# Kernel optimization log

Hardware: AMD Instinct MI355X
Metric: run time of the kernel (lower is better)

Reference implementation:

```python
import jax, jax.numpy as jnp
import numpy as np

B, N, F, H, L = 2048, 64, 128, 2, 3
Dh = F // H          # feats per head
E = 7                # 3 diff + 1 dist + 3 sigmoid shifts
MAX_SPECIES = 100
SHIFTS = (2.0, 4.0, 6.0)
NEG = -1e9


def layernorm(x):
    # no_upscale_ln: plain normalization, unit scale, zero offset
    m = x.mean(-1, keepdims=True)
    v = x.var(-1, keepdims=True)
    return (x - m) * jax.lax.rsqrt(v + 1e-5)


def featurize(diffs):
    # featurize_real_space_vector with sigmoid_shifts=[2,4,6]
    d = jnp.sqrt((diffs * diffs).sum(-1, keepdims=True) + 1e-12)  # [B,N,N,1]
    sig = jnp.concatenate([jax.nn.sigmoid(d - s) for s in SHIFTS], -1)
    return jnp.concatenate([diffs, d, sig], -1)  # [B,N,N,E]


def setup_inputs() -> dict:
    key = jax.random.key(0)
    ks = jax.random.split(key, 12)
    s = 0.05
    coords = jax.random.normal(ks[0], (B, N, 3), jnp.float32) * 3.0
    species = jax.random.randint(ks[1], (B, N), 1, MAX_SPECIES + 1, jnp.int32)
    lengths = jax.random.randint(ks[2], (B,), N // 2, N + 1)
    mask = jnp.arange(N)[None, :] < lengths[:, None]  # [B,N] bool, padded tails
    return {
        "coords": coords,
        "species": species,
        "mask": mask,
        "embed": jax.random.normal(ks[3], (MAX_SPECIES, F), jnp.float32) * s,
        "Wq": jax.random.normal(ks[4], (L, F, F), jnp.float32) * s,
        "Wk": jax.random.normal(ks[5], (L, F, F), jnp.float32) * s,
        "Wv": jax.random.normal(ks[6], (L, F, F), jnp.float32) * s,
        "Wo": jax.random.normal(ks[7], (L, F, F), jnp.float32) * s,
        "We": jax.random.normal(ks[8], (L, E, H), jnp.float32) * s,
        "Wf": jax.random.normal(ks[9], (L, F, F), jnp.float32) * s,
        "bf": jnp.zeros((L, F), jnp.float32),
    }


def _forward(coords, embed, Wq, Wk, Wv, Wo, We, Wf, bf, species, mask):
    # initial node features from species embedding (species is 1-based)
    h = embed[species - 1] * mask[..., None].astype(embed.dtype)  # [B,N,F]
    nn_mask = mask[:, :, None] & mask[:, None, :]                  # [B,N,N]
    diffs = coords[:, :, None, :] - coords[:, None, :, :]          # [B,N,N,3]
    edges = featurize(diffs) * nn_mask[..., None].astype(coords.dtype)  # [B,N,N,E]
    inv_sqrt_dh = 1.0 / np.sqrt(Dh).astype(np.float32)
    for l in range(L):
        hn = layernorm(h)
        q = (hn @ Wq[l]).reshape(B, N, H, Dh)
        k = (hn @ Wk[l]).reshape(B, N, H, Dh)
        v = (hn @ Wv[l]).reshape(B, N, H, Dh)
        logits = jnp.einsum("bnhd,bmhd->bhnm", q, k) * inv_sqrt_dh
        logits = logits + jnp.einsum("bnme,eh->bhnm", edges, We[l])
        logits = jnp.where(nn_mask[:, None], logits, NEG)
        attn = jax.nn.softmax(logits, axis=-1)                     # [B,H,N,N]
        msg = jnp.einsum("bhnm,bmhd->bnhd", attn, v).reshape(B, N, F)
        h = h + msg @ Wo[l]                                        # attention residual
        h = h + jnp.tanh(layernorm(h) @ Wf[l] + bf[l])             # PsiformerDense residual
        h = h * mask[..., None].astype(h.dtype)
    return layernorm(h)


def reference(coords, species, mask, embed, Wq, Wk, Wv, Wo, We, Wf, bf):
    return _forward(coords, embed, Wq, Wk, Wv, Wo, We, Wf, bf, species, mask)
```

## Files before the change

### kernel.cpp

```cpp
#include <hip/hip_runtime.h>


#define NBATCH 2048
#define NATOM  64
#define NF     128
#define NLAYER 3
#define STR    132
#define ASTRB  136
#define VSTR   72
#define NTH    512

using bf16x8 = __attribute__((ext_vector_type(8))) __bf16;
using bf16x4 = __attribute__((ext_vector_type(4))) __bf16;
using f32x4  = __attribute__((ext_vector_type(4))) float;

__device__ __forceinline__ float bf2f(unsigned short u) {
    union { unsigned int i; float f; } v; v.i = ((unsigned int)u) << 16; return v.f;
}
__device__ __forceinline__ unsigned short f2bf(float f) {
    union { float ff; unsigned int i; } v; v.ff = f;
    unsigned int x = v.i;
    if ((x & 0x7f800000u) == 0x7f800000u) return (unsigned short)(x >> 16);
    return (unsigned short)((x + 0x7fffu + ((x >> 16) & 1u)) >> 16);
}
__device__ __forceinline__ unsigned short bfbits(float x) {
    union { __bf16 b; unsigned short u; } v; v.b = (__bf16)x; return v.u;
}

__device__ __forceinline__ float fast_rcp(float x)  { return __builtin_amdgcn_rcpf(x); }
__device__ __forceinline__ float fast_sqrt(float x) { return __builtin_amdgcn_sqrtf(x); }
__device__ __forceinline__ float fast_exp(float x)  { return __builtin_amdgcn_exp2f(x * 1.4426950408889634f); }

template<bool BF16>
__device__ __forceinline__ float ldT(const void* p, int i) {
    if constexpr (BF16) return bf2f(((const unsigned short*)p)[i]);
    else                return ((const float*)p)[i];
}
template<bool BF16>
__device__ __forceinline__ float4 ld4T(const void* p, int i) {
    if constexpr (BF16) {
        ushort4 v = *(const ushort4*)((const unsigned short*)p + i);
        return make_float4(bf2f(v.x), bf2f(v.y), bf2f(v.z), bf2f(v.w));
    } else {
        return *(const float4*)((const float*)p + i);
    }
}

__device__ __forceinline__ void ln_stats(const float (&h)[4][4], float (&mu)[4], float (&rs)[4]) {
    #pragma unroll
    for (int i = 0; i < 4; ++i) {
        float s  = h[i][0] + h[i][1] + h[i][2] + h[i][3];
        float s2 = h[i][0]*h[i][0] + h[i][1]*h[i][1] + h[i][2]*h[i][2] + h[i][3]*h[i][3];
        #pragma unroll
        for (int m = 1; m <= 16; m <<= 1) {
            s  += __shfl_xor(s,  m);
            s2 += __shfl_xor(s2, m);
        }
        float mm = s * (1.f / 128.f);
        float vv = s2 * (1.f / 128.f) - mm * mm;
        mu[i] = mm;
        rs[i] = rsqrtf(fmaxf(vv, 0.f) + 1e-5f);
    }
}

__device__ __forceinline__ void write_a(const float (&h)[4][4], const float (&mu)[4], const float (&rs)[4],
                                        __bf16* __restrict__ a_hi, int r0, int fq) {
    #pragma unroll
    for (int i = 0; i < 4; ++i) {
        bf16x4 v;
        #pragma unroll
        for (int jj = 0; jj < 4; ++jj)
            v[jj] = (__bf16)((h[i][jj] - mu[i]) * rs[i]);
        *(bf16x4*)&a_hi[(r0 + i) * ASTRB + fq * 4] = v;
    }
}

template<bool WLO>
__device__ __forceinline__ void mfma_dense(const __bf16* __restrict__ a_hi,
                                           const __bf16* __restrict__ bp,
                                           f32x4 (&acc)[2][2], int lane, int wave)
{
    const int R0  = (wave >> 2) << 5;
    const int Cq2 = (wave & 3) << 1;
    const int c = lane & 15, g = lane >> 4;
    const __bf16* bl = bp + 16384;
    #pragma unroll
    for (int t2 = 0; t2 < 2; ++t2)
        #pragma unroll
        for (int j = 0; j < 2; ++j)
            acc[t2][j] = (f32x4){0.f, 0.f, 0.f, 0.f};
    #pragma unroll
    for (int kc = 0; kc < 4; ++kc) {
        const int ao = kc * 32 + (g << 3);
        bf16x8 a0h = *(const bf16x8*)&a_hi[(R0 + c) * ASTRB + ao];
        bf16x8 a1h = *(const bf16x8*)&a_hi[(R0 + 16 + c) * ASTRB + ao];
        #pragma unroll
        for (int j = 0; j < 2; ++j) {
            const int bi = ((((kc << 3) + Cq2 + j) << 6) + lane) << 3;
            bf16x8 bh = *(const bf16x8*)&bp[bi];
            acc[0][j] = __builtin_amdgcn_mfma_f32_16x16x32_bf16(a0h, bh, acc[0][j], 0, 0, 0);
            acc[1][j] = __builtin_amdgcn_mfma_f32_16x16x32_bf16(a1h, bh, acc[1][j], 0, 0, 0);
            if constexpr (WLO) {
                bf16x8 bv = *(const bf16x8*)&bl[bi];
                acc[0][j] = __builtin_amdgcn_mfma_f32_16x16x32_bf16(a0h, bv, acc[0][j], 0, 0, 0);
                acc[1][j] = __builtin_amdgcn_mfma_f32_16x16x32_bf16(a1h, bv, acc[1][j], 0, 0, 0);
            }
        }
    }
}

__device__ __forceinline__ void writeC_rm(const f32x4 (&acc)[2][2],
                                          __bf16* __restrict__ hi, int lane, int wave)
{
    const int R0 = (wave >> 2) << 5;
    const int C0 = (wave & 3) << 5;
    const int c = lane & 15, g4 = (lane >> 4) << 2;
    #pragma unroll
    for (int t2 = 0; t2 < 2; ++t2)
    #pragma unroll
    for (int j = 0; j < 2; ++j)
    #pragma unroll
    for (int r = 0; r < 4; ++r)
        hi[(R0 + 16*t2 + g4 + r) * ASTRB + C0 + 16*j + c] = (__bf16)acc[t2][j][r];
}

__device__ __forceinline__ void writeC_vt(const f32x4 (&acc)[2][2],
                                          __bf16* __restrict__ hi, int lane, int wave)
{
    const int R0 = (wave >> 2) << 5;
    const int C0 = (wave & 3) << 5;
    const int c = lane & 15, g4 = (lane >> 4) << 2;
    #pragma unroll
    for (int t2 = 0; t2 < 2; ++t2)
    #pragma unroll
    for (int j = 0; j < 2; ++j)
    #pragma unroll
    for (int r = 0; r < 4; ++r) {
        int m = R0 + 16*t2 + g4 + r, d = C0 + 16*j + c;
        hi[d * VSTR + m] = (__bf16)acc[t2][j][r];
    }
}

__device__ __forceinline__ void writeC_f32(const f32x4 (&acc)[2][2],
                                           float* __restrict__ dst, int lane, int wave)
{
    const int R0 = (wave >> 2) << 5;
    const int C0 = (wave & 3) << 5;
    const int c = lane & 15, g4 = (lane >> 4) << 2;
    #pragma unroll
    for (int t2 = 0; t2 < 2; ++t2)
    #pragma unroll
    for (int j = 0; j < 2; ++j)
    #pragma unroll
    for (int r = 0; r < 4; ++r)
        dst[(R0 + 16*t2 + g4 + r) * STR + C0 + 16*j + c] = acc[t2][j][r];
}

template<bool BF16>
__global__ __launch_bounds__(256)
void prep_w(const void* __restrict__ Wq, const void* __restrict__ Wk,
            const void* __restrict__ Wv, const void* __restrict__ Wo,
            const void* __restrict__ Wf, unsigned short* __restrict__ wpack)
{
    {
        const unsigned int* w = (const unsigned int*)Wq;
        bool isbf = true;
        #pragma unroll
        for (int i = 0; i < 16; ++i) {
            unsigned int e = (w[i] >> 7) & 0xFFu;
            isbf = isbf && (e >= 0x60u && e <= 0x7Eu);
        }
        if (isbf != BF16) return;
    }
    const int mat  = blockIdx.x;
    const int kind = mat / 3, l = mat % 3;
    const void* src = (kind == 0) ? Wq : (kind == 1) ? Wk : (kind == 2) ? Wv
                    : (kind == 3) ? Wo : Wf;
    unsigned short* dh = wpack + (size_t)mat * 32768;
    unsigned short* dl = dh + 16384;
    for (int f = threadIdx.x; f < 16384; f += 256) {
        int e    = f & 7;
        int lane = (f >> 3) & 63;
        int tj   = (f >> 9) & 7;
        int kc   = f >> 12;
        int row  = kc * 32 + ((lane >> 4) << 3) + e;
        int col  = tj * 16 + (lane & 15);
        float x  = ldT<BF16>(src, (l * NF + row) * NF + col);
        unsigned short hi = f2bf(x);
        unsigned short lo = f2bf(x - bf2f(hi));
        dh[f] = hi; dl[f] = lo;
    }
}

static constexpr size_t SMEM_BYTES =
    (size_t)26624 * 2 + (256 + 48) * 4 + 16;

template<bool BF16>
__global__ __launch_bounds__(NTH, 2)
void gnn_fused(const void* __restrict__ coords,
               const int* __restrict__ species,
               const unsigned char* __restrict__ maskraw,
               const void* __restrict__ embed,
               const void* __restrict__ Wq,
               const void* __restrict__ We,
               const void* __restrict__ bfb,
               const unsigned short* __restrict__ wpack,
               void* __restrict__ out)
{
    constexpr bool WLO = !BF16;
    {
        const unsigned int* w = (const unsigned int*)Wq;
        bool isbf = true;
        #pragma unroll
        for (int i = 0; i < 16; ++i) {
            unsigned int e = (w[i] >> 7) & 0xFFu;
            isbf = isbf && (e >= 0x60u && e <= 0x7Eu);
        }
        if (isbf != BF16) return;
    }

    extern __shared__ __bf16 sm[];
    __bf16* a_hi  = sm;
    __bf16* k_hi  = sm + 8704;
    __bf16* vt_hi = sm + 17408;
    float*  scratch = (float*)k_hi;
    float*  tailf = (float*)(sm + 26624);
    float*  cs   = tailf;
    float*  wel  = cs + 256;
    int*    lenp = (int*)(wel + 48);

    const int t    = threadIdx.x;
    const int b    = blockIdx.x;
    const int fq   = t & 31;
    const int r0   = (t >> 5) * 4;
    const int lane = t & 63;
    const int wave = t >> 6;
    const int c    = lane & 15;
    const int g    = lane >> 4;
    const int g4   = g << 2;
    const int hd   = wave >> 2;
    const int wb   = (wave & 3) << 4;

    if (t < 64) {
        cs[t * 4 + 0] = ldT<BF16>(coords, (b * NATOM + t) * 3 + 0);
        cs[t * 4 + 1] = ldT<BF16>(coords, (b * NATOM + t) * 3 + 1);
        cs[t * 4 + 2] = ldT<BF16>(coords, (b * NATOM + t) * 3 + 2);
    }
    if (t >= 64 && t < 64 + 42) wel[t - 64] = ldT<BF16>(We, t - 64);
    if (t < 64) {
        unsigned int w0 = *(const unsigned int*)maskraw;
        bool f;
        if (w0 == 1u)               f = ((const int*)maskraw)[b * NATOM + t] != 0;
        else if (w0 == 0x01010101u) f = maskraw[b * NATOM + t] != 0;
        else if (w0 == 0x3F800000u) f = ((const float*)maskraw)[b * NATOM + t] != 0.f;
        else                        f = ((const unsigned short*)maskraw)[b * NATOM + t] != 0;
        unsigned long long bal = __ballot(f);
        if (t == 0) *lenp = (int)__popcll(bal);
    }

    float h[4][4];
    #pragma unroll
    for (int i = 0; i < 4; ++i) {
        int sp = species[b * NATOM + r0 + i];
        float4 ev = ld4T<BF16>(embed, (sp - 1) * NF + fq * 4);
        h[i][0] = ev.x; h[i][1] = ev.y; h[i][2] = ev.z; h[i][3] = ev.w;
    }
    __syncthreads();
    const int len = *lenp;
    #pragma unroll
    for (int i = 0; i < 4; ++i)
        if (r0 + i >= len) { h[i][0]=0.f; h[i][1]=0.f; h[i][2]=0.f; h[i][3]=0.f; }

    float mu[4], rs[4];
    for (int l = 0; l < NLAYER; ++l) {
        ln_stats(h, mu, rs);
        write_a(h, mu, rs, a_hi, r0, fq);
        __syncthreads();

        {
            f32x4 kacc[2][2];
            mfma_dense<WLO>(a_hi, (const __bf16*)wpack + (size_t)(3 + l) * 32768, kacc, lane, wave);
            writeC_rm(kacc, k_hi, lane, wave);
        }
        {
            f32x4 vacc[2][2];
            mfma_dense<WLO>(a_hi, (const __bf16*)wpack + (size_t)(6 + l) * 32768, vacc, lane, wave);
            writeC_vt(vacc, vt_hi, lane, wave);
        }
        f32x4 qacc[2][2];
        mfma_dense<WLO>(a_hi, (const __bf16*)wpack + (size_t)(0 + l) * 32768, qacc, lane, wave);
        __syncthreads();
        writeC_rm(qacc, a_hi, lane, wave);
        __syncthreads();

        f32x4 lacc[4];
        #pragma unroll
        for (int jt = 0; jt < 4; ++jt) lacc[jt] = (f32x4){0.f,0.f,0.f,0.f};
        #pragma unroll
        for (int kc = 0; kc < 2; ++kc) {
            const int qo = (wb + c) * ASTRB + hd * 64 + kc * 32 + (g << 3);
            bf16x8 qh = *(const bf16x8*)&a_hi[qo];
            #pragma unroll
            for (int jt = 0; jt < 4; ++jt) {
                const int ko = (jt * 16 + c) * ASTRB + hd * 64 + kc * 32 + (g << 3);
                bf16x8 kh = *(const bf16x8*)&k_hi[ko];
                lacc[jt] = __builtin_amdgcn_mfma_f32_16x16x32_bf16(qh, kh, lacc[jt], 0, 0, 0);
            }
        }
        __syncthreads();

        float we_[7];
        #pragma unroll
        for (int e = 0; e < 7; ++e) we_[e] = wel[l * 14 + e * 2 + hd];
        float cnx[4], cny[4], cnz[4];
        #pragma unroll
        for (int r = 0; r < 4; ++r) {
            int n = wb + g4 + r;
            cnx[r] = cs[n*4]; cny[r] = cs[n*4+1]; cnz[r] = cs[n*4+2];
        }
        float lg[4][4];
        #pragma unroll
        for (int jt = 0; jt < 4; ++jt) {
            int mc = jt * 16 + c;
            float cmx = cs[mc*4], cmy = cs[mc*4+1], cmz = cs[mc*4+2];
            #pragma unroll
            for (int r = 0; r < 4; ++r) {
                float dx = cnx[r]-cmx, dy = cny[r]-cmy, dz = cnz[r]-cmz;
                float d  = fast_sqrt(dx*dx + dy*dy + dz*dz + 1e-12f);
                float et = fast_exp(-d);
                float s1 = fast_rcp(1.f + 7.38905609893065f   * et);
                float s2 = fast_rcp(1.f + 54.598150033144236f * et);
                float s3 = fast_rcp(1.f + 403.4287934927351f  * et);
                lg[jt][r] = lacc[jt][r] * 0.125f
                          + dx*we_[0] + dy*we_[1] + dz*we_[2] + d*we_[3]
                          + s1*we_[4] + s2*we_[5] + s3*we_[6];
            }
        }
        float mx[4] = {-3e38f, -3e38f, -3e38f, -3e38f};
        #pragma unroll
        for (int jt = 0; jt < 4; ++jt)
            if (jt * 16 + c < len) {
                #pragma unroll
                for (int r = 0; r < 4; ++r) mx[r] = fmaxf(mx[r], lg[jt][r]);
            }
        #pragma unroll
        for (int r = 0; r < 4; ++r) {
            mx[r] = fmaxf(mx[r], __shfl_xor(mx[r], 1));
            mx[r] = fmaxf(mx[r], __shfl_xor(mx[r], 2));
            mx[r] = fmaxf(mx[r], __shfl_xor(mx[r], 4));
            mx[r] = fmaxf(mx[r], __shfl_xor(mx[r], 8));
        }
        float sv[4] = {0.f, 0.f, 0.f, 0.f};
        #pragma unroll
        for (int jt = 0; jt < 4; ++jt) {
            bool vm = (jt * 16 + c) < len;
            #pragma unroll
            for (int r = 0; r < 4; ++r) {
                float e = vm ? fast_exp(lg[jt][r] - mx[r]) : 0.f;
                lg[jt][r] = e; sv[r] += e;
            }
        }
        #pragma unroll
        for (int r = 0; r < 4; ++r) {
            sv[r] += __shfl_xor(sv[r], 1);
            sv[r] += __shfl_xor(sv[r], 2);
            sv[r] += __shfl_xor(sv[r], 4);
            sv[r] += __shfl_xor(sv[r], 8);
        }
        float inv[4];
        #pragma unroll
        for (int r = 0; r < 4; ++r)
            inv[r] = (wb + g4 + r < len) ? fast_rcp(sv[r]) : 0.f;

        {
            char* pw = (char*)k_hi + wave * 2048;
            #pragma unroll
            for (int jt = 0; jt < 4; ++jt)
                #pragma unroll
                for (int r = 0; r < 4; ++r) {
                    int x = g4 + r, mm = jt * 16 + c;
                    *(__bf16*)(pw + x * 128 + ((mm * 2) ^ ((x & 7) << 4))) =
                        (__bf16)(lg[jt][r] * inv[r]);
                }
        }

        f32x4 macc[4];
        #pragma unroll
        for (int jt = 0; jt < 4; ++jt) macc[jt] = (f32x4){0.f,0.f,0.f,0.f};
        #pragma unroll
        for (int kc = 0; kc < 2; ++kc) {
            const char* pw = (const char*)k_hi + wave * 2048;
            const int m0 = kc * 32 + (g << 3);
            bf16x8 ph = *(const bf16x8*)(pw + c * 128 + ((m0 * 2) ^ ((c & 7) << 4)));
            #pragma unroll
            for (int jt = 0; jt < 4; ++jt) {
                const int vo = (hd * 64 + jt * 16 + c) * VSTR + kc * 32 + (g << 3);
                bf16x8 vh = *(const bf16x8*)&vt_hi[vo];
                macc[jt] = __builtin_amdgcn_mfma_f32_16x16x32_bf16(ph, vh, macc[jt], 0, 0, 0);
            }
        }
        #pragma unroll
        for (int jt = 0; jt < 4; ++jt)
            #pragma unroll
            for (int r = 0; r < 4; ++r) {
                int idx = (wb + g4 + r) * ASTRB + hd * 64 + jt * 16 + c;
                a_hi[idx] = (__bf16)macc[jt][r];
            }
        __syncthreads();

        {
            f32x4 oacc[2][2];
            mfma_dense<WLO>(a_hi, (const __bf16*)wpack + (size_t)(9 + l) * 32768, oacc, lane, wave);
            writeC_f32(oacc, scratch, lane, wave);
        }
        __syncthreads();
        #pragma unroll
        for (int i = 0; i < 4; ++i) {
            float4 ov = *(const float4*)&scratch[(r0 + i) * STR + fq * 4];
            h[i][0] += ov.x; h[i][1] += ov.y; h[i][2] += ov.z; h[i][3] += ov.w;
        }

        ln_stats(h, mu, rs);
        write_a(h, mu, rs, a_hi, r0, fq);
        __syncthreads();
        {
            f32x4 facc[2][2];
            mfma_dense<WLO>(a_hi, (const __bf16*)wpack + (size_t)(12 + l) * 32768, facc, lane, wave);
            writeC_f32(facc, scratch, lane, wave);
        }
        __syncthreads();
        {
            float4 bv = ld4T<BF16>(bfb, l * NF + fq * 4);
            #pragma unroll
            for (int i = 0; i < 4; ++i) {
                float z0 = scratch[(r0 + i) * STR + fq * 4 + 0] + bv.x;
                float z1 = scratch[(r0 + i) * STR + fq * 4 + 1] + bv.y;
                float z2 = scratch[(r0 + i) * STR + fq * 4 + 2] + bv.z;
                float z3 = scratch[(r0 + i) * STR + fq * 4 + 3] + bv.w;
                h[i][0] += 1.f - 2.f * fast_rcp(fast_exp(2.f*z0) + 1.f);
                h[i][1] += 1.f - 2.f * fast_rcp(fast_exp(2.f*z1) + 1.f);
                h[i][2] += 1.f - 2.f * fast_rcp(fast_exp(2.f*z2) + 1.f);
                h[i][3] += 1.f - 2.f * fast_rcp(fast_exp(2.f*z3) + 1.f);
            }
        }
        #pragma unroll
        for (int i = 0; i < 4; ++i)
            if (r0 + i >= len) { h[i][0]=0.f; h[i][1]=0.f; h[i][2]=0.f; h[i][3]=0.f; }
    }

    ln_stats(h, mu, rs);
    #pragma unroll
    for (int i = 0; i < 4; ++i) {
        int idx = b * NATOM * NF + (r0 + i) * NF + fq * 4;
        float o0 = (h[i][0]-mu[i])*rs[i], o1 = (h[i][1]-mu[i])*rs[i];
        float o2 = (h[i][2]-mu[i])*rs[i], o3 = (h[i][3]-mu[i])*rs[i];
        if constexpr (BF16) {
            ushort4 o;
            o.x = bfbits(o0); o.y = bfbits(o1); o.z = bfbits(o2); o.w = bfbits(o3);
            *(ushort4*)((unsigned short*)out + idx) = o;
        } else {
            *(float4*)((float*)out + idx) = make_float4(o0, o1, o2, o3);
        }
    }
}

extern "C" void kernel_launch(void* const* d_in, const int* in_sizes, int n_in,
                              void* d_out, int out_size, void* d_ws, size_t ws_size,
                              hipStream_t stream) {
    const void*           coords  = d_in[0];
    const int*            species = (const int*)d_in[1];
    const unsigned char*  maskraw = (const unsigned char*)d_in[2];
    const void*           embed   = d_in[3];
    const void*           Wq      = d_in[4];
    const void*           Wk      = d_in[5];
    const void*           Wv      = d_in[6];
    const void*           Wo      = d_in[7];
    const void*           We      = d_in[8];
    const void*           Wf      = d_in[9];
    const void*           bfb     = d_in[10];

    unsigned short* wpack = (unsigned short*)d_ws;

    (void)hipFuncSetAttribute((const void*)gnn_fused<true>,
                              hipFuncAttributeMaxDynamicSharedMemorySize,
                              (int)SMEM_BYTES);
    (void)hipFuncSetAttribute((const void*)gnn_fused<false>,
                              hipFuncAttributeMaxDynamicSharedMemorySize,
                              (int)SMEM_BYTES);

    prep_w<true ><<<dim3(15), dim3(256), 0, stream>>>(Wq, Wk, Wv, Wo, Wf, wpack);
    prep_w<false><<<dim3(15), dim3(256), 0, stream>>>(Wq, Wk, Wv, Wo, Wf, wpack);

    gnn_fused<true ><<<dim3(NBATCH), dim3(NTH), SMEM_BYTES, stream>>>(
        coords, species, maskraw, embed, Wq, We, bfb, wpack, d_out);
    gnn_fused<false><<<dim3(NBATCH), dim3(NTH), SMEM_BYTES, stream>>>(
        coords, species, maskraw, embed, Wq, We, bfb, wpack, d_out);
}
```

Measured before the change: 446.0 us.

## Process two molecules per block to reuse weight fragments across MFMAs

Each workgroup now handles two molecules. Every dense projection loads each packed weight fragment once and feeds it to MFMAs for both molecules, which halves global weight traffic per molecule and gives more independent MFMA chains to interleave. The cost is doubled LDS use and roughly doubled register state. Launch bounds drop from 2 to 1 workgroup per CU, so occupancy may fall and latency hiding may suffer.

After: 500.9 us. 1.12x slower.

```diff
diff --git a/kernel.cpp b/kernel.cpp
--- a/kernel.cpp
+++ b/kernel.cpp
@@ -9,6 +9,8 @@
 #define ASTRB  136
 #define VSTR   72
 #define NTH    512
+#define MOLS   2
+#define MOLELT 26624
 
 using bf16x8 = __attribute__((ext_vector_type(8))) __bf16;
 using bf16x4 = __attribute__((ext_vector_type(4))) __bf16;
@@ -76,34 +78,43 @@
 }
 
 template<bool WLO>
-__device__ __forceinline__ void mfma_dense(const __bf16* __restrict__ a_hi,
-                                           const __bf16* __restrict__ bp,
-                                           f32x4 (&acc)[2][2], int lane, int wave)
+__device__ __forceinline__ void mfma_dense2(const __bf16* __restrict__ a0,
+                                            const __bf16* __restrict__ a1,
+                                            const __bf16* __restrict__ bp,
+                                            f32x4 (&acc)[MOLS][2][2], int lane, int wave)
 {
     const int R0  = (wave >> 2) << 5;
     const int Cq2 = (wave & 3) << 1;
     const int c = lane & 15, g = lane >> 4;
     const __bf16* bl = bp + 16384;
     #pragma unroll
-    for (int t2 = 0; t2 < 2; ++t2)
-        #pragma unroll
-        for (int j = 0; j < 2; ++j)
-            acc[t2][j] = (f32x4){0.f, 0.f, 0.f, 0.f};
+    for (int m = 0; m < MOLS; ++m)
+        #pragma unroll
+        for (int t2 = 0; t2 < 2; ++t2)
+            #pragma unroll
+            for (int j = 0; j < 2; ++j)
+                acc[m][t2][j] = (f32x4){0.f, 0.f, 0.f, 0.f};
     #pragma unroll
     for (int kc = 0; kc < 4; ++kc) {
         const int ao = kc * 32 + (g << 3);
-        bf16x8 a0h = *(const bf16x8*)&a_hi[(R0 + c) * ASTRB + ao];
-        bf16x8 a1h = *(const bf16x8*)&a_hi[(R0 + 16 + c) * ASTRB + ao];
+        bf16x8 a00 = *(const bf16x8*)&a0[(R0 + c) * ASTRB + ao];
+        bf16x8 a01 = *(const bf16x8*)&a0[(R0 + 16 + c) * ASTRB + ao];
+        bf16x8 a10 = *(const bf16x8*)&a1[(R0 + c) * ASTRB + ao];
+        bf16x8 a11 = *(const bf16x8*)&a1[(R0 + 16 + c) * ASTRB + ao];
         #pragma unroll
         for (int j = 0; j < 2; ++j) {
             const int bi = ((((kc << 3) + Cq2 + j) << 6) + lane) << 3;
             bf16x8 bh = *(const bf16x8*)&bp[bi];
-            acc[0][j] = __builtin_amdgcn_mfma_f32_16x16x32_bf16(a0h, bh, acc[0][j], 0, 0, 0);
-            acc[1][j] = __builtin_amdgcn_mfma_f32_16x16x32_bf16(a1h, bh, acc[1][j], 0, 0, 0);
+            acc[0][0][j] = __builtin_amdgcn_mfma_f32_16x16x32_bf16(a00, bh, acc[0][0][j], 0, 0, 0);
+            acc[1][0][j] = __builtin_amdgcn_mfma_f32_16x16x32_bf16(a10, bh, acc[1][0][j], 0, 0, 0);
+            acc[0][1][j] = __builtin_amdgcn_mfma_f32_16x16x32_bf16(a01, bh, acc[0][1][j], 0, 0, 0);
+            acc[1][1][j] = __builtin_amdgcn_mfma_f32_16x16x32_bf16(a11, bh, acc[1][1][j], 0, 0, 0);
             if constexpr (WLO) {
                 bf16x8 bv = *(const bf16x8*)&bl[bi];
-                acc[0][j] = __builtin_amdgcn_mfma_f32_16x16x32_bf16(a0h, bv, acc[0][j], 0, 0, 0);
-                acc[1][j] = __builtin_amdgcn_mfma_f32_16x16x32_bf16(a1h, bv, acc[1][j], 0, 0, 0);
+                acc[0][0][j] = __builtin_amdgcn_mfma_f32_16x16x32_bf16(a00, bv, acc[0][0][j], 0, 0, 0);
+                acc[1][0][j] = __builtin_amdgcn_mfma_f32_16x16x32_bf16(a10, bv, acc[1][0][j], 0, 0, 0);
+                acc[0][1][j] = __builtin_amdgcn_mfma_f32_16x16x32_bf16(a01, bv, acc[0][1][j], 0, 0, 0);
+                acc[1][1][j] = __builtin_amdgcn_mfma_f32_16x16x32_bf16(a11, bv, acc[1][1][j], 0, 0, 0);
             }
         }
     }
@@ -193,10 +204,10 @@
 }
 
 static constexpr size_t SMEM_BYTES =
-    (size_t)26624 * 2 + (256 + 48) * 4 + 16;
+    (size_t)MOLS * MOLELT * 2 + (MOLS * 256 + 48) * 4 + 16;
 
 template<bool BF16>
-__global__ __launch_bounds__(NTH, 2)
+__global__ __launch_bounds__(NTH, 1)
 void gnn_fused(const void* __restrict__ coords,
                const int* __restrict__ species,
                const unsigned char* __restrict__ maskraw,
@@ -220,14 +231,20 @@
     }
 
     extern __shared__ __bf16 sm[];
-    __bf16* a_hi  = sm;
-    __bf16* k_hi  = sm + 8704;
-    __bf16* vt_hi = sm + 17408;
-    float*  scratch = (float*)k_hi;
-    float*  tailf = (float*)(sm + 26624);
-    float*  cs   = tailf;
-    float*  wel  = cs + 256;
-    int*    lenp = (int*)(wel + 48);
+    __bf16 *a_hi[MOLS], *k_hi[MOLS], *vt_hi[MOLS];
+    float  *scratch[MOLS], *csp[MOLS];
+    float* tailf = (float*)(sm + MOLS * MOLELT);
+    #pragma unroll
+    for (int m = 0; m < MOLS; ++m) {
+        __bf16* base = sm + m * MOLELT;
+        a_hi[m]  = base;
+        k_hi[m]  = base + 8704;
+        vt_hi[m] = base + 17408;
+        scratch[m] = (float*)k_hi[m];
+        csp[m] = tailf + m * 256;
+    }
+    float* wel  = tailf + MOLS * 256;
+    int*   lenp = (int*)(wel + 48);
 
     const int t    = threadIdx.x;
     const int b    = blockIdx.x;
@@ -241,225 +258,263 @@
     const int hd   = wave >> 2;
     const int wb   = (wave & 3) << 4;
 
-    if (t < 64) {
-        cs[t * 4 + 0] = ldT<BF16>(coords, (b * NATOM + t) * 3 + 0);
-        cs[t * 4 + 1] = ldT<BF16>(coords, (b * NATOM + t) * 3 + 1);
-        cs[t * 4 + 2] = ldT<BF16>(coords, (b * NATOM + t) * 3 + 2);
-    }
-    if (t >= 64 && t < 64 + 42) wel[t - 64] = ldT<BF16>(We, t - 64);
-    if (t < 64) {
+    if (t < 64 * MOLS) {
+        int tl = t & 63;
+        float* csm = tailf + (t >> 6) * 256;
+        int gi = (b * MOLS + (t >> 6)) * NATOM + tl;
+        csm[tl * 4 + 0] = ldT<BF16>(coords, gi * 3 + 0);
+        csm[tl * 4 + 1] = ldT<BF16>(coords, gi * 3 + 1);
+        csm[tl * 4 + 2] = ldT<BF16>(coords, gi * 3 + 2);
+    }
+    if (t >= 64 * MOLS && t < 64 * MOLS + 42) wel[t - 64 * MOLS] = ldT<BF16>(We, t - 64 * MOLS);
+    if (t < 64 * MOLS) {
+        int tl = t & 63, mm = t >> 6;
+        int gi = (b * MOLS + mm) * NATOM + tl;
         unsigned int w0 = *(const unsigned int*)maskraw;
         bool f;
-        if (w0 == 1u)               f = ((const int*)maskraw)[b * NATOM + t] != 0;
-        else if (w0 == 0x01010101u) f = maskraw[b * NATOM + t] != 0;
-        else if (w0 == 0x3F800000u) f = ((const float*)maskraw)[b * NATOM + t] != 0.f;
-        else                        f = ((const unsigned short*)maskraw)[b * NATOM + t] != 0;
+        if (w0 == 1u)               f = ((const int*)maskraw)[gi] != 0;
+        else if (w0 == 0x01010101u) f = maskraw[gi] != 0;
+        else if (w0 == 0x3F800000u) f = ((const float*)maskraw)[gi] != 0.f;
+        else                        f = ((const unsigned short*)maskraw)[gi] != 0;
         unsigned long long bal = __ballot(f);
-        if (t == 0) *lenp = (int)__popcll(bal);
-    }
-
-    float h[4][4];
-    #pragma unroll
-    for (int i = 0; i < 4; ++i) {
-        int sp = species[b * NATOM + r0 + i];
-        float4 ev = ld4T<BF16>(embed, (sp - 1) * NF + fq * 4);
-        h[i][0] = ev.x; h[i][1] = ev.y; h[i][2] = ev.z; h[i][3] = ev.w;
-    }
+        if (tl == 0) lenp[mm] = (int)__popcll(bal);
+    }
+
+    float h[MOLS][4][4];
+    #pragma unroll
+    for (int m = 0; m < MOLS; ++m)
+        #pragma unroll
+        for (int i = 0; i < 4; ++i) {
+            int sp = species[(b * MOLS + m) * NATOM + r0 + i];
+            float4 ev = ld4T<BF16>(embed, (sp - 1) * NF + fq * 4);
+            h[m][i][0] = ev.x; h[m][i][1] = ev.y; h[m][i][2] = ev.z; h[m][i][3] = ev.w;
+        }
     __syncthreads();
-    const int len = *lenp;
-    #pragma unroll
-    for (int i = 0; i < 4; ++i)
-        if (r0 + i >= len) { h[i][0]=0.f; h[i][1]=0.f; h[i][2]=0.f; h[i][3]=0.f; }
+    int len[MOLS];
+    #pragma unroll
+    for (int m = 0; m < MOLS; ++m) len[m] = lenp[m];
+    #pragma unroll
+    for (int m = 0; m < MOLS; ++m)
+        #pragma unroll
+        for (int i = 0; i < 4; ++i)
+            if (r0 + i >= len[m]) { h[m][i][0]=0.f; h[m][i][1]=0.f; h[m][i][2]=0.f; h[m][i][3]=0.f; }
 
     float mu[4], rs[4];
     for (int l = 0; l < NLAYER; ++l) {
-        ln_stats(h, mu, rs);
-        write_a(h, mu, rs, a_hi, r0, fq);
+        #pragma unroll
+        for (int m = 0; m < MOLS; ++m) {
+            ln_stats(h[m], mu, rs);
+            write_a(h[m], mu, rs, a_hi[m], r0, fq);
+        }
         __syncthreads();
 
         {
-            f32x4 kacc[2][2];
-            mfma_dense<WLO>(a_hi, (const __bf16*)wpack + (size_t)(3 + l) * 32768, kacc, lane, wave);
-            writeC_rm(kacc, k_hi, lane, wave);
+            f32x4 kacc[MOLS][2][2];
+            mfma_dense2<WLO>(a_hi[0], a_hi[1], (const __bf16*)wpack + (size_t)(3 + l) * 32768, kacc, lane, wave);
+            writeC_rm(kacc[0], k_hi[0], lane, wave);
+            writeC_rm(kacc[1], k_hi[1], lane, wave);
         }
         {
-            f32x4 vacc[2][2];
-            mfma_dense<WLO>(a_hi, (const __bf16*)wpack + (size_t)(6 + l) * 32768, vacc, lane, wave);
-            writeC_vt(vacc, vt_hi, lane, wave);
-        }
-        f32x4 qacc[2][2];
-        mfma_dense<WLO>(a_hi, (const __bf16*)wpack + (size_t)(0 + l) * 32768, qacc, lane, wave);
-        __syncthreads();
-        writeC_rm(qacc, a_hi, lane, wave);
-        __syncthreads();
-
-        f32x4 lacc[4];
-        #pragma unroll
-        for (int jt = 0; jt < 4; ++jt) lacc[jt] = (f32x4){0.f,0.f,0.f,0.f};
-        #pragma unroll
-        for (int kc = 0; kc < 2; ++kc) {
-            const int qo = (wb + c) * ASTRB + hd * 64 + kc * 32 + (g << 3);
-            bf16x8 qh = *(const bf16x8*)&a_hi[qo];
+            f32x4 vacc[MOLS][2][2];
+            mfma_dense2<WLO>(a_hi[0], a_hi[1], (const __bf16*)wpack + (size_t)(6 + l) * 32768, vacc, lane, wave);
+            writeC_vt(vacc[0], vt_hi[0], lane, wave);
+            writeC_vt(vacc[1], vt_hi[1], lane, wave);
+        }
+        f32x4 qacc[MOLS][2][2];
+        mfma_dense2<WLO>(a_hi[0], a_hi[1], (const __bf16*)wpack + (size_t)(0 + l) * 32768, qacc, lane, wave);
+        __syncthreads();
+        writeC_rm(qacc[0], a_hi[0], lane, wave);
+        writeC_rm(qacc[1], a_hi[1], lane, wave);
+        __syncthreads();
+
+        f32x4 lacc[MOLS][4];
+        #pragma unroll
+        for (int m = 0; m < MOLS; ++m) {
+            #pragma unroll
+            for (int jt = 0; jt < 4; ++jt) lacc[m][jt] = (f32x4){0.f,0.f,0.f,0.f};
+            #pragma unroll
+            for (int kc = 0; kc < 2; ++kc) {
+                const int qo = (wb + c) * ASTRB + hd * 64 + kc * 32 + (g << 3);
+                bf16x8 qh = *(const bf16x8*)&a_hi[m][qo];
+                #pragma unroll
+                for (int jt = 0; jt < 4; ++jt) {
+                    const int ko = (jt * 16 + c) * ASTRB + hd * 64 + kc * 32 + (g << 3);
+                    bf16x8 kh = *(const bf16x8*)&k_hi[m][ko];
+                    lacc[m][jt] = __builtin_amdgcn_mfma_f32_16x16x32_bf16(qh, kh, lacc[m][jt], 0, 0, 0);
+                }
+            }
+        }
+        __syncthreads();
+
+        float we_[7];
+        #pragma unroll
+        for (int e = 0; e < 7; ++e) we_[e] = wel[l * 14 + e * 2 + hd];
+        #pragma unroll
+        for (int m = 0; m < MOLS; ++m) {
+            float* cs = csp[m];
+            float cnx[4], cny[4], cnz[4];
+            #pragma unroll
+            for (int r = 0; r < 4; ++r) {
+                int n = wb + g4 + r;
+                cnx[r] = cs[n*4]; cny[r] = cs[n*4+1]; cnz[r] = cs[n*4+2];
+            }
+            float lg[4][4];
             #pragma unroll
             for (int jt = 0; jt < 4; ++jt) {
-                const int ko = (jt * 16 + c) * ASTRB + hd * 64 + kc * 32 + (g << 3);
-                bf16x8 kh = *(const bf16x8*)&k_hi[ko];
-                lacc[jt] = __builtin_amdgcn_mfma_f32_16x16x32_bf16(qh, kh, lacc[jt], 0, 0, 0);
-            }
-        }
-        __syncthreads();
-
-        float we_[7];
-        #pragma unroll
-        for (int e = 0; e < 7; ++e) we_[e] = wel[l * 14 + e * 2 + hd];
-        float cnx[4], cny[4], cnz[4];
-        #pragma unroll
-        for (int r = 0; r < 4; ++r) {
-            int n = wb + g4 + r;
-            cnx[r] = cs[n*4]; cny[r] = cs[n*4+1]; cnz[r] = cs[n*4+2];
-        }
-        float lg[4][4];
-        #pragma unroll
-        for (int jt = 0; jt < 4; ++jt) {
-            int mc = jt * 16 + c;
-            float cmx = cs[mc*4], cmy = cs[mc*4+1], cmz = cs[mc*4+2];
+                int mc = jt * 16 + c;
+                float cmx = cs[mc*4], cmy = cs[mc*4+1], cmz = cs[mc*4+2];
+                #pragma unroll
+                for (int r = 0; r < 4; ++r) {
+                    float dx = cnx[r]-cmx, dy = cny[r]-cmy, dz = cnz[r]-cmz;
+                    float d  = fast_sqrt(dx*dx + dy*dy + dz*dz + 1e-12f);
+                    float et = fast_exp(-d);
+                    float s1 = fast_rcp(1.f + 7.38905609893065f   * et);
+                    float s2 = fast_rcp(1.f + 54.598150033144236f * et);
+                    float s3 = fast_rcp(1.f + 403.4287934927351f  * et);
+                    lg[jt][r] = lacc[m][jt][r] * 0.125f
+                              + dx*we_[0] + dy*we_[1] + dz*we_[2] + d*we_[3]
+                              + s1*we_[4] + s2*we_[5] + s3*we_[6];
+                }
+            }
+            float mx[4] = {-3e38f, -3e38f, -3e38f, -3e38f};
+            #pragma unroll
+            for (int jt = 0; jt < 4; ++jt)
+                if (jt * 16 + c < len[m]) {
+                    #pragma unroll
+                    for (int r = 0; r < 4; ++r) mx[r] = fmaxf(mx[r], lg[jt][r]);
+                }
             #pragma unroll
             for (int r = 0; r < 4; ++r) {
-                float dx = cnx[r]-cmx, dy = cny[r]-cmy, dz = cnz[r]-cmz;
-                float d  = fast_sqrt(dx*dx + dy*dy + dz*dz + 1e-12f);
-                float et = fast_exp(-d);
-                float s1 = fast_rcp(1.f + 7.38905609893065f   * et);
-                float s2 = fast_rcp(1.f + 54.598150033144236f * et);
-                float s3 = fast_rcp(1.f + 403.4287934927351f  * et);
-                lg[jt][r] = lacc[jt][r] * 0.125f
-                          + dx*we_[0] + dy*we_[1] + dz*we_[2] + d*we_[3]
-                          + s1*we_[4] + s2*we_[5] + s3*we_[6];
-            }
-        }
-        float mx[4] = {-3e38f, -3e38f, -3e38f, -3e38f};
-        #pragma unroll
-        for (int jt = 0; jt < 4; ++jt)
-            if (jt * 16 + c < len) {
-                #pragma unroll
-                for (int r = 0; r < 4; ++r) mx[r] = fmaxf(mx[r], lg[jt][r]);
-            }
-        #pragma unroll
-        for (int r = 0; r < 4; ++r) {
-            mx[r] = fmaxf(mx[r], __shfl_xor(mx[r], 1));
-            mx[r] = fmaxf(mx[r], __shfl_xor(mx[r], 2));
-            mx[r] = fmaxf(mx[r], __shfl_xor(mx[r], 4));
-            mx[r] = fmaxf(mx[r], __shfl_xor(mx[r], 8));
-        }
-        float sv[4] = {0.f, 0.f, 0.f, 0.f};
-        #pragma unroll
-        for (int jt = 0; jt < 4; ++jt) {
-            bool vm = (jt * 16 + c) < len;
+                mx[r] = fmaxf(mx[r], __shfl_xor(mx[r], 1));
+                mx[r] = fmaxf(mx[r], __shfl_xor(mx[r], 2));
+                mx[r] = fmaxf(mx[r], __shfl_xor(mx[r], 4));
+                mx[r] = fmaxf(mx[r], __shfl_xor(mx[r], 8));
+            }
+            float sv[4] = {0.f, 0.f, 0.f, 0.f};
+            #pragma unroll
+            for (int jt = 0; jt < 4; ++jt) {
+                bool vm = (jt * 16 + c) < len[m];
+                #pragma unroll
+                for (int r = 0; r < 4; ++r) {
+                    float e = vm ? fast_exp(lg[jt][r] - mx[r]) : 0.f;
+                    lg[jt][r] = e; sv[r] += e;
+                }
+            }
             #pragma unroll
             for (int r = 0; r < 4; ++r) {
-                float e = vm ? fast_exp(lg[jt][r] - mx[r]) : 0.f;
-                lg[jt][r] = e; sv[r] += e;
-            }
-        }
-        #pragma unroll
-        for (int r = 0; r < 4; ++r) {
-            sv[r] += __shfl_xor(sv[r], 1);
-            sv[r] += __shfl_xor(sv[r], 2);
-            sv[r] += __shfl_xor(sv[r], 4);
-            sv[r] += __shfl_xor(sv[r], 8);
-        }
-        float inv[4];
-        #pragma unroll
-        for (int r = 0; r < 4; ++r)
-            inv[r] = (wb + g4 + r < len) ? fast_rcp(sv[r]) : 0.f;
+                sv[r] += __shfl_xor(sv[r], 1);
+                sv[r] += __shfl_xor(sv[r], 2);
+                sv[r] += __shfl_xor(sv[r], 4);
+                sv[r] += __shfl_xor(sv[r], 8);
+            }
+            float inv[4];
+            #pragma unroll
+            for (int r = 0; r < 4; ++r)
+                inv[r] = (wb + g4 + r < len[m]) ? fast_rcp(sv[r]) : 0.f;
+
+            {
+                char* pw = (char*)k_hi[m] + wave * 2048;
+                #pragma unroll
+                for (int jt = 0; jt < 4; ++jt)
+                    #pragma unroll
+                    for (int r = 0; r < 4; ++r) {
+                        int x = g4 + r, mm2 = jt * 16 + c;
+                        *(__bf16*)(pw + x * 128 + ((mm2 * 2) ^ ((x & 7) << 4))) =
+                            (__bf16)(lg[jt][r] * inv[r]);
+                    }
+            }
+
+            f32x4 macc[4];
+            #pragma unroll
+            for (int jt = 0; jt < 4; ++jt) macc[jt] = (f32x4){0.f,0.f,0.f,0.f};
+            #pragma unroll
+            for (int kc = 0; kc < 2; ++kc) {
+                const char* pw = (const char*)k_hi[m] + wave * 2048;
+                const int m0 = kc * 32 + (g << 3);
+                bf16x8 ph = *(const bf16x8*)(pw + c * 128 + ((m0 * 2) ^ ((c & 7) << 4)));
+                #pragma unroll
+                for (int jt = 0; jt < 4; ++jt) {
+                    const int vo = (hd * 64 + jt * 16 + c) * VSTR + kc * 32 + (g << 3);
+                    bf16x8 vh = *(const bf16x8*)&vt_hi[m][vo];
+                    macc[jt] = __builtin_amdgcn_mfma_f32_16x16x32_bf16(ph, vh, macc[jt], 0, 0, 0);
+                }
+            }
+            #pragma unroll
+            for (int jt = 0; jt < 4; ++jt)
+                #pragma unroll
+                for (int r = 0; r < 4; ++r) {
+                    int idx = (wb + g4 + r) * ASTRB + hd * 64 + jt * 16 + c;
+                    a_hi[m][idx] = (__bf16)macc[jt][r];
+                }
+        }
+        __syncthreads();
 
         {
-            char* pw = (char*)k_hi + wave * 2048;
-            #pragma unroll
-            for (int jt = 0; jt < 4; ++jt)
-                #pragma unroll
-                for (int r = 0; r < 4; ++r) {
-                    int x = g4 + r, mm = jt * 16 + c;
-                    *(__bf16*)(pw + x * 128 + ((mm * 2) ^ ((x & 7) << 4))) =
-                        (__bf16)(lg[jt][r] * inv[r]);
-                }
-        }
-
-        f32x4 macc[4];
-        #pragma unroll
-        for (int jt = 0; jt < 4; ++jt) macc[jt] = (f32x4){0.f,0.f,0.f,0.f};
-        #pragma unroll
-        for (int kc = 0; kc < 2; ++kc) {
-            const char* pw = (const char*)k_hi + wave * 2048;
-            const int m0 = kc * 32 + (g << 3);
-            bf16x8 ph = *(const bf16x8*)(pw + c * 128 + ((m0 * 2) ^ ((c & 7) << 4)));
-            #pragma unroll
-            for (int jt = 0; jt < 4; ++jt) {
-                const int vo = (hd * 64 + jt * 16 + c) * VSTR + kc * 32 + (g << 3);
-                bf16x8 vh = *(const bf16x8*)&vt_hi[vo];
-                macc[jt] = __builtin_amdgcn_mfma_f32_16x16x32_bf16(ph, vh, macc[jt], 0, 0, 0);
-            }
-        }
-        #pragma unroll
-        for (int jt = 0; jt < 4; ++jt)
-            #pragma unroll
-            for (int r = 0; r < 4; ++r) {
-                int idx = (wb + g4 + r) * ASTRB + hd * 64 + jt * 16 + c;
-                a_hi[idx] = (__bf16)macc[jt][r];
-            }
-        __syncthreads();
-
+            f32x4 oacc[MOLS][2][2];
+            mfma_dense2<WLO>(a_hi[0], a_hi[1], (const __bf16*)wpack + (size_t)(9 + l) * 32768, oacc, lane, wave);
+            writeC_f32(oacc[0], scratch[0], lane, wave);
+            writeC_f32(oacc[1], scratch[1], lane, wave);
+        }
+        __syncthreads();
+        #pragma unroll
+        for (int m = 0; m < MOLS; ++m)
+            #pragma unroll
+            for (int i = 0; i < 4; ++i) {
+                float4 ov = *(const float4*)&scratch[m][(r0 + i) * STR + fq * 4];
+                h[m][i][0] += ov.x; h[m][i][1] += ov.y; h[m][i][2] += ov.z; h[m][i][3] += ov.w;
+            }
+
+        #pragma unroll
+        for (int m = 0; m < MOLS; ++m) {
+            ln_stats(h[m], mu, rs);
+            write_a(h[m], mu, rs, a_hi[m], r0, fq);
+        }
+        __syncthreads();
         {
-            f32x4 oacc[2][2];
-            mfma_dense<WLO>(a_hi, (const __bf16*)wpack + (size_t)(9 + l) * 32768, oacc, lane, wave);
-            writeC_f32(oacc, scratch, lane, wave);
-        }
-        __syncthreads();
-        #pragma unroll
-        for (int i = 0; i < 4; ++i) {
-            float4 ov = *(const float4*)&scratch[(r0 + i) * STR + fq * 4];
-            h[i][0] += ov.x; h[i][1] += ov.y; h[i][2] += ov.z; h[i][3] += ov.w;
-        }
-
-        ln_stats(h, mu, rs);
-        write_a(h, mu, rs, a_hi, r0, fq);
-        __syncthreads();
-        {
-            f32x4 facc[2][2];
-            mfma_dense<WLO>(a_hi, (const __bf16*)wpack + (size_t)(12 + l) * 32768, facc, lane, wave);
-            writeC_f32(facc, scratch, lane, wave);
+            f32x4 facc[MOLS][2][2];
+            mfma_dense2<WLO>(a_hi[0], a_hi[1], (const __bf16*)wpack + (size_t)(12 + l) * 32768, facc, lane, wave);
+            writeC_f32(facc[0], scratch[0], lane, wave);
+            writeC_f32(facc[1], scratch[1], lane, wave);
         }
         __syncthreads();
         {
             float4 bv = ld4T<BF16>(bfb, l * NF + fq * 4);
             #pragma unroll
-            for (int i = 0; i < 4; ++i) {
-                float z0 = scratch[(r0 + i) * STR + fq * 4 + 0] + bv.x;
-                float z1 = scratch[(r0 + i) * STR + fq * 4 + 1] + bv.y;
-                float z2 = scratch[(r0 + i) * STR + fq * 4 + 2] + bv.z;
-                float z3 = scratch[(r0 + i) * STR + fq * 4 + 3] + bv.w;
-                h[i][0] += 1.f - 2.f * fast_rcp(fast_exp(2.f*z0) + 1.f);
-                h[i][1] += 1.f - 2.f * fast_rcp(fast_exp(2.f*z1) + 1.f);
-                h[i][2] += 1.f - 2.f * fast_rcp(fast_exp(2.f*z2) + 1.f);
-                h[i][3] += 1.f - 2.f * fast_rcp(fast_exp(2.f*z3) + 1.f);
-            }
-        }
-        #pragma unroll
-        for (int i = 0; i < 4; ++i)
-            if (r0 + i >= len) { h[i][0]=0.f; h[i][1]=0.f; h[i][2]=0.f; h[i][3]=0.f; }
-    }
-
-    ln_stats(h, mu, rs);
-    #pragma unroll
-    for (int i = 0; i < 4; ++i) {
-        int idx = b * NATOM * NF + (r0 + i) * NF + fq * 4;
-        float o0 = (h[i][0]-mu[i])*rs[i], o1 = (h[i][1]-mu[i])*rs[i];
-        float o2 = (h[i][2]-mu[i])*rs[i], o3 = (h[i][3]-mu[i])*rs[i];
-        if constexpr (BF16) {
-            ushort4 o;
-            o.x = bfbits(o0); o.y = bfbits(o1); o.z = bfbits(o2); o.w = bfbits(o3);
-            *(ushort4*)((unsigned short*)out + idx) = o;
-        } else {
-            *(float4*)((float*)out + idx) = make_float4(o0, o1, o2, o3);
+            for (int m = 0; m < MOLS; ++m)
+                #pragma unroll
+                for (int i = 0; i < 4; ++i) {
+                    float z0 = scratch[m][(r0 + i) * STR + fq * 4 + 0] + bv.x;
+                    float z1 = scratch[m][(r0 + i) * STR + fq * 4 + 1] + bv.y;
+                    float z2 = scratch[m][(r0 + i) * STR + fq * 4 + 2] + bv.z;
+                    float z3 = scratch[m][(r0 + i) * STR + fq * 4 + 3] + bv.w;
+                    h[m][i][0] += 1.f - 2.f * fast_rcp(fast_exp(2.f*z0) + 1.f);
+                    h[m][i][1] += 1.f - 2.f * fast_rcp(fast_exp(2.f*z1) + 1.f);
+                    h[m][i][2] += 1.f - 2.f * fast_rcp(fast_exp(2.f*z2) + 1.f);
+                    h[m][i][3] += 1.f - 2.f * fast_rcp(fast_exp(2.f*z3) + 1.f);
+                }
+        }
+        #pragma unroll
+        for (int m = 0; m < MOLS; ++m)
+            #pragma unroll
+            for (int i = 0; i < 4; ++i)
+                if (r0 + i >= len[m]) { h[m][i][0]=0.f; h[m][i][1]=0.f; h[m][i][2]=0.f; h[m][i][3]=0.f; }
+    }
+
+    #pragma unroll
+    for (int m = 0; m < MOLS; ++m) {
+        ln_stats(h[m], mu, rs);
+        #pragma unroll
+        for (int i = 0; i < 4; ++i) {
+            int idx = (b * MOLS + m) * NATOM * NF + (r0 + i) * NF + fq * 4;
+            float o0 = (h[m][i][0]-mu[i])*rs[i], o1 = (h[m][i][1]-mu[i])*rs[i];
+            float o2 = (h[m][i][2]-mu[i])*rs[i], o3 = (h[m][i][3]-mu[i])*rs[i];
+            if constexpr (BF16) {
+                ushort4 o;
+                o.x = bfbits(o0); o.y = bfbits(o1); o.z = bfbits(o2); o.w = bfbits(o3);
+                *(ushort4*)((unsigned short*)out + idx) = o;
+            } else {
+                *(float4*)((float*)out + idx) = make_float4(o0, o1, o2, o3);
+            }
         }
     }
 }
@@ -491,8 +546,8 @@
     prep_w<true ><<<dim3(15), dim3(256), 0, stream>>>(Wq, Wk, Wv, Wo, Wf, wpack);
     prep_w<false><<<dim3(15), dim3(256), 0, stream>>>(Wq, Wk, Wv, Wo, Wf, wpack);
 
-    gnn_fused<true ><<<dim3(NBATCH), dim3(NTH), SMEM_BYTES, stream>>>(
+    gnn_fused<true ><<<dim3(NBATCH / MOLS), dim3(NTH), SMEM_BYTES, stream>>>(
         coords, species, maskraw, embed, Wq, We, bfb, wpack, d_out);
-    gnn_fused<false><<<dim3(NBATCH), dim3(NTH), SMEM_BYTES, stream>>>(
+    gnn_fused<false><<<dim3(NBATCH / MOLS), dim3(NTH), SMEM_BYTES, stream>>>(
         coords, species, maskraw, embed, Wq, We, bfb, wpack, d_out);
 }
```

## Give Q and P their own LDS buffers, drop barriers, hoist distance/exp out of layer loop

Applied to the files above, without the earlier changes.

Q and the per-wave softmax probabilities now live in dedicated shared-memory regions instead of aliasing a_hi and k_hi. That removes two block-wide barriers per layer. Pairwise distances and exp(-d) are computed once before the layer loop and kept in registers, where they were previously recomputed every layer. Shared memory grows from about 53 KB to about 87 KB, launch bounds drop to one block per CU, and the 32 extra live registers per thread may hurt occupancy and latency hiding.

Measured after the change: 422.3 us. -5.3%, faster.

```diff
diff --git a/kernel.cpp b/kernel.cpp
--- a/kernel.cpp
+++ b/kernel.cpp
@@ -193,10 +193,10 @@
 }
 
 static constexpr size_t SMEM_BYTES =
-    (size_t)26624 * 2 + (256 + 48) * 4 + 16;
+    (size_t)43520 * 2 + (256 + 48) * 4 + 16;
 
 template<bool BF16>
-__global__ __launch_bounds__(NTH, 2)
+__global__ __launch_bounds__(NTH, 1)
 void gnn_fused(const void* __restrict__ coords,
                const int* __restrict__ species,
                const unsigned char* __restrict__ maskraw,
@@ -221,10 +221,12 @@
 
     extern __shared__ __bf16 sm[];
     __bf16* a_hi  = sm;
-    __bf16* k_hi  = sm + 8704;
-    __bf16* vt_hi = sm + 17408;
+    __bf16* q_hi  = sm + 8704;
+    __bf16* k_hi  = sm + 17408;
+    __bf16* vt_hi = sm + 26112;
+    __bf16* p_hi  = sm + 35328;
     float*  scratch = (float*)k_hi;
-    float*  tailf = (float*)(sm + 26624);
+    float*  tailf = (float*)(sm + 43520);
     float*  cs   = tailf;
     float*  wel  = cs + 256;
     int*    lenp = (int*)(wel + 48);
@@ -271,6 +273,28 @@
     for (int i = 0; i < 4; ++i)
         if (r0 + i >= len) { h[i][0]=0.f; h[i][1]=0.f; h[i][2]=0.f; h[i][3]=0.f; }
 
+    float pdc[4][4], pec[4][4];
+    {
+        float cnx[4], cny[4], cnz[4];
+        #pragma unroll
+        for (int r = 0; r < 4; ++r) {
+            int n = wb + g4 + r;
+            cnx[r] = cs[n*4]; cny[r] = cs[n*4+1]; cnz[r] = cs[n*4+2];
+        }
+        #pragma unroll
+        for (int jt = 0; jt < 4; ++jt) {
+            int mc = jt * 16 + c;
+            float cmx = cs[mc*4], cmy = cs[mc*4+1], cmz = cs[mc*4+2];
+            #pragma unroll
+            for (int r = 0; r < 4; ++r) {
+                float dx = cnx[r]-cmx, dy = cny[r]-cmy, dz = cnz[r]-cmz;
+                float d = fast_sqrt(dx*dx + dy*dy + dz*dz + 1e-12f);
+                pdc[jt][r] = d;
+                pec[jt][r] = fast_exp(-d);
+            }
+        }
+    }
+
     float mu[4], rs[4];
     for (int l = 0; l < NLAYER; ++l) {
         ln_stats(h, mu, rs);
@@ -287,10 +311,11 @@
             mfma_dense<WLO>(a_hi, (const __bf16*)wpack + (size_t)(6 + l) * 32768, vacc, lane, wave);
             writeC_vt(vacc, vt_hi, lane, wave);
         }
-        f32x4 qacc[2][2];
-        mfma_dense<WLO>(a_hi, (const __bf16*)wpack + (size_t)(0 + l) * 32768, qacc, lane, wave);
-        __syncthreads();
-        writeC_rm(qacc, a_hi, lane, wave);
+        {
+            f32x4 qacc[2][2];
+            mfma_dense<WLO>(a_hi, (const __bf16*)wpack + (size_t)(0 + l) * 32768, qacc, lane, wave);
+            writeC_rm(qacc, q_hi, lane, wave);
+        }
         __syncthreads();
 
         f32x4 lacc[4];
@@ -299,7 +324,7 @@
         #pragma unroll
         for (int kc = 0; kc < 2; ++kc) {
             const int qo = (wb + c) * ASTRB + hd * 64 + kc * 32 + (g << 3);
-            bf16x8 qh = *(const bf16x8*)&a_hi[qo];
+            bf16x8 qh = *(const bf16x8*)&q_hi[qo];
             #pragma unroll
             for (int jt = 0; jt < 4; ++jt) {
                 const int ko = (jt * 16 + c) * ASTRB + hd * 64 + kc * 32 + (g << 3);
@@ -307,7 +332,6 @@
                 lacc[jt] = __builtin_amdgcn_mfma_f32_16x16x32_bf16(qh, kh, lacc[jt], 0, 0, 0);
             }
         }
-        __syncthreads();
 
         float we_[7];
         #pragma unroll
@@ -326,13 +350,13 @@
             #pragma unroll
             for (int r = 0; r < 4; ++r) {
                 float dx = cnx[r]-cmx, dy = cny[r]-cmy, dz = cnz[r]-cmz;
-                float d  = fast_sqrt(dx*dx + dy*dy + dz*dz + 1e-12f);
-                float et = fast_exp(-d);
+                float et = pec[jt][r];
                 float s1 = fast_rcp(1.f + 7.38905609893065f   * et);
                 float s2 = fast_rcp(1.f + 54.598150033144236f * et);
                 float s3 = fast_rcp(1.f + 403.4287934927351f  * et);
                 lg[jt][r] = lacc[jt][r] * 0.125f
-                          + dx*we_[0] + dy*we_[1] + dz*we_[2] + d*we_[3]
+                          + dx*we_[0] + dy*we_[1] + dz*we_[2]
+                          + pdc[jt][r]*we_[3]
                           + s1*we_[4] + s2*we_[5] + s3*we_[6];
             }
         }
@@ -373,7 +397,7 @@
             inv[r] = (wb + g4 + r < len) ? fast_rcp(sv[r]) : 0.f;
 
         {
-            char* pw = (char*)k_hi + wave * 2048;
+            char* pw = (char*)p_hi + wave * 2048;
             #pragma unroll
             for (int jt = 0; jt < 4; ++jt)
                 #pragma unroll
@@ -389,7 +413,7 @@
         for (int jt = 0; jt < 4; ++jt) macc[jt] = (f32x4){0.f,0.f,0.f,0.f};
         #pragma unroll
         for (int kc = 0; kc < 2; ++kc) {
-            const char* pw = (const char*)k_hi + wave * 2048;
+            const char* pw = (const char*)p_hi + wave * 2048;
             const int m0 = kc * 32 + (g << 3);
             bf16x8 ph = *(const bf16x8*)(pw + c * 128 + ((m0 * 2) ^ ((c & 7) << 4)));
             #pragma unroll
```
